# Optimization experiments

Measured on AMD Instinct MI355X. Metric: run time of the kernel, lower is better.

The kernel has to match this reference:

```python
import jax, jax.numpy as jnp
import numpy as np

N, F_IN, HID, NH1, NCLS = 8192, 256, 64, 4, 16
LRELU_ALPHA = 0.2  # tf.nn.leaky_relu default


def setup_inputs() -> dict:
    key = jax.random.key(0)
    ks = jax.random.split(key, 12)
    s = 0.05
    seq = jax.random.normal(ks[0], (1, N, F_IN), jnp.float32)
    # sparse-ish adjacency -> additive mask bias (0 on edges, -1e9 elsewhere)
    adj = jax.random.uniform(ks[1], (N, N)) < 0.005
    adj = adj | jnp.eye(N, dtype=bool)
    bias_mat = jnp.where(adj, 0.0, -1e9).astype(jnp.float32)[None]  # [1,N,N]
    return {
        "seq": seq,
        "bias_mat": bias_mat,
        "W1": jax.random.normal(ks[2], (NH1, F_IN, HID), jnp.float32) * s,
        "a1_src": jax.random.normal(ks[3], (NH1, HID, 1), jnp.float32) * s,
        "a1_dst": jax.random.normal(ks[4], (NH1, HID, 1), jnp.float32) * s,
        "b1_src": jnp.zeros((NH1, 1), jnp.float32),
        "b1_dst": jnp.zeros((NH1, 1), jnp.float32),
        "bias1": jnp.zeros((NH1, HID), jnp.float32),
        "W2": jax.random.normal(ks[5], (1, NH1 * HID, NCLS), jnp.float32) * s,
        "a2_src": jax.random.normal(ks[6], (1, NCLS, 1), jnp.float32) * s,
        "a2_dst": jax.random.normal(ks[7], (1, NCLS, 1), jnp.float32) * s,
        "b2_src": jnp.zeros((1, 1), jnp.float32),
        "b2_dst": jnp.zeros((1, 1), jnp.float32),
        "bias2": jnp.zeros((1, NCLS), jnp.float32),
    }


def _gat_layer(x, bias_mat, W, a_src, a_dst, b_src, b_dst, bias_out):
    # x: [N, Fin]; W: [nh, Fin, H]; bias_mat: [1, N, N]
    fts = jnp.einsum('nf,hfd->hnd', x, W)                      # Conv1D(k=1, no bias)
    f1 = jnp.einsum('hnd,hdo->hno', fts, a_src) + b_src[:, None, :]  # [nh,N,1]
    f2 = jnp.einsum('hnd,hdo->hno', fts, a_dst) + b_dst[:, None, :]  # [nh,N,1]
    logits = f1 + jnp.swapaxes(f2, 1, 2)                       # [nh,N,N]
    coefs = jax.nn.softmax(jax.nn.leaky_relu(logits, LRELU_ALPHA) + bias_mat, axis=-1)
    vals = jnp.einsum('hnm,hmd->hnd', coefs, fts)              # [nh,N,H]
    return vals + bias_out[:, None, :]


def reference(seq, bias_mat, W1, a1_src, a1_dst, b1_src, b1_dst, bias1,
              W2, a2_src, a2_dst, b2_src, b2_dst, bias2):
    x = seq[0]  # [N, F_IN]; batch dim is 1
    # layer 1: NH1 heads, elu activation, concat over heads
    h = jax.nn.elu(_gat_layer(x, bias_mat, W1, a1_src, a1_dst, b1_src, b1_dst, bias1))
    h1 = jnp.transpose(h, (1, 0, 2)).reshape(N, NH1 * HID)     # tf.concat(heads, -1)
    # output layer: 1 head, identity activation, averaged over final heads (=1)
    out = _gat_layer(h1, bias_mat, W2, a2_src, a2_dst, b2_src, b2_dst, bias2)
    logits = out[0] / 1.0                                      # add_n/final_sum
    return logits[None]  # [1, N, NCLS]
```

## Files before the change

### kernel.cpp

```cpp
#include <hip/hip_runtime.h>
#include <hip/hip_bf16.h>
#include <math.h>

#define NN    8192
#define FIN   256
#define HID   64
#define NH    4
#define NC    16
#define MAXD  128
#define ALPHA 0.2f
#define KC    32

typedef float nfloat4 __attribute__((ext_vector_type(4)));
__device__ __forceinline__ float4 ldnt4(const float4* p) {
    nfloat4 v = __builtin_nontemporal_load((const nfloat4*)p);
    return make_float4(v.x, v.y, v.z, v.w);
}
__device__ __forceinline__ ushort f2bf(float x) {
    __hip_bfloat16 h = __float2bfloat16(x);
    return *reinterpret_cast<ushort*>(&h);
}
__device__ __forceinline__ float bfhi(unsigned u) { return __uint_as_float(u & 0xffff0000u); }
__device__ __forceinline__ float bflo(unsigned u) { return __uint_as_float(u << 16); }

__device__ __forceinline__ void scan_row(
    int row, int lane, int* colsW,
    const float* __restrict__ bias, int* __restrict__ deg, int* __restrict__ cols)
{
    const unsigned long long lt = (1ull << lane) - 1ull;
    colsW[lane] = 0; colsW[64 + lane] = 0;
    const float4* rp = (const float4*)(bias + (size_t)row * NN);
    float4 vv[8];
    #pragma unroll
    for (int k = 0; k < 8; ++k) vv[k] = ldnt4(rp + k*64 + lane);
    int base = 0;
    #pragma unroll
    for (int s = 0; s < 4; ++s) {
        #pragma unroll
        for (int k = 0; k < 8; ++k) {
            const float4 v = vv[k];
            if (s < 3) vv[k] = ldnt4(rp + ((s+1)*8 + k)*64 + lane);
            const unsigned long long m0 = __ballot(v.x == 0.f);
            const unsigned long long m1 = __ballot(v.y == 0.f);
            const unsigned long long m2 = __ballot(v.z == 0.f);
            const unsigned long long m3 = __ballot(v.w == 0.f);
            const int cb = ((s*8 + k)*64 + lane)*4;
            int p = base + __popcll(m0&lt) + __popcll(m1&lt)
                         + __popcll(m2&lt) + __popcll(m3&lt);
            if (v.x == 0.f) { if (p < MAXD) colsW[p] = cb;     ++p; }
            if (v.y == 0.f) { if (p < MAXD) colsW[p] = cb + 1; ++p; }
            if (v.z == 0.f) { if (p < MAXD) colsW[p] = cb + 2; ++p; }
            if (v.w == 0.f) { if (p < MAXD) colsW[p] = cb + 3; ++p; }
            base += __popcll(m0) + __popcll(m1) + __popcll(m2) + __popcll(m3);
        }
    }
    const int d = base < MAXD ? base : MAXD;
    if (lane == 0) deg[row] = d;
    cols[(size_t)row*MAXD + lane]      = colsW[lane];
    cols[(size_t)row*MAXD + 64 + lane] = colsW[64 + lane];
}

__global__ __launch_bounds__(256) void k_gemm_scan(
    const float* __restrict__ seq, const float* __restrict__ W1,
    const float* __restrict__ a1s, const float* __restrict__ a1d,
    const float* __restrict__ b1s, const float* __restrict__ b1d,
    const float* __restrict__ bias,
    ushort* __restrict__ fts1g, float* __restrict__ f1v, float* __restrict__ f2v,
    int* __restrict__ deg, int* __restrict__ cols)
{
    __shared__ union {
        struct { float xsT[KC][68]; float w[KC][68]; } g;
        struct { float r1[64][17];  float r2[64][17]; } gr;
        int colsS[4][MAXD];
    } S;
    const int t = threadIdx.x, bid = blockIdx.x;
    const int w = t >> 6, lane = t & 63;

    const bool isGemm = (bid < 1024) && !(bid & 1);
    if (!isGemm) {
        const int si = (bid < 1024) ? (bid >> 1) : (bid - 512);
        scan_row(si*4 + w, lane, &S.colsS[w][0], bias, deg, cols);
        return;
    }
    const int gi = bid >> 1;
    const int head = gi & 3, rowbase = (gi >> 2) * 64;
    const int tr = t >> 4, tc = t & 15;

    float acc[4][4] = {};
    for (int kc = 0; kc < FIN / KC; ++kc) {
        #pragma unroll
        for (int i = 0; i < 2; ++i) {
            const int lin = t + i*256;
            const int row = lin >> 3, kq = lin & 7;
            const float4 v = *(const float4*)(seq + (size_t)(rowbase + row)*FIN + kc*KC + kq*4);
            S.g.xsT[kq*4+0][row] = v.x;
            S.g.xsT[kq*4+1][row] = v.y;
            S.g.xsT[kq*4+2][row] = v.z;
            S.g.xsT[kq*4+3][row] = v.w;
        }
        #pragma unroll
        for (int i = 0; i < 2; ++i) {
            const int lin = t + i*256;
            const int k = lin >> 4, dq = lin & 15;
            *(float4*)&S.g.w[k][dq*4] =
                *(const float4*)(W1 + ((size_t)head*FIN + kc*KC + k)*HID + dq*4);
        }
        __syncthreads();
        #pragma unroll 8
        for (int k = 0; k < KC; ++k) {
            const float4 aa = *(const float4*)&S.g.xsT[k][tr*4];
            const float4 bb = *(const float4*)&S.g.w[k][tc*4];
            acc[0][0] += aa.x*bb.x; acc[0][1] += aa.x*bb.y; acc[0][2] += aa.x*bb.z; acc[0][3] += aa.x*bb.w;
            acc[1][0] += aa.y*bb.x; acc[1][1] += aa.y*bb.y; acc[1][2] += aa.y*bb.z; acc[1][3] += aa.y*bb.w;
            acc[2][0] += aa.z*bb.x; acc[2][1] += aa.z*bb.y; acc[2][2] += aa.z*bb.z; acc[2][3] += aa.z*bb.w;
            acc[3][0] += aa.w*bb.x; acc[3][1] += aa.w*bb.y; acc[3][2] += aa.w*bb.z; acc[3][3] += aa.w*bb.w;
        }
        __syncthreads();
    }
    float p1[4], p2[4];
    #pragma unroll
    for (int i = 0; i < 4; ++i) {
        const int node = rowbase + tr*4 + i;
        ushort4 o;
        o.x = f2bf(acc[i][0]); o.y = f2bf(acc[i][1]);
        o.z = f2bf(acc[i][2]); o.w = f2bf(acc[i][3]);
        *(ushort4*)&fts1g[(size_t)node*(NH*HID) + head*HID + tc*4] = o;
        float s1 = 0.f, s2 = 0.f;
        #pragma unroll
        for (int j = 0; j < 4; ++j) {
            s1 += acc[i][j] * a1s[head*HID + tc*4 + j];
            s2 += acc[i][j] * a1d[head*HID + tc*4 + j];
        }
        p1[i] = s1; p2[i] = s2;
    }
    #pragma unroll
    for (int i = 0; i < 4; ++i) {
        S.gr.r1[tr*4 + i][tc] = p1[i];
        S.gr.r2[tr*4 + i][tc] = p2[i];
    }
    __syncthreads();
    if (t < 64) {
        float s1 = b1s[head], s2 = b1d[head];
        #pragma unroll
        for (int q = 0; q < 16; ++q) { s1 += S.gr.r1[t][q]; s2 += S.gr.r2[t][q]; }
        f1v[(rowbase + t)*NH + head] = s1;
        f2v[(rowbase + t)*NH + head] = s2;
    }
}

__global__ __launch_bounds__(256) void k_attn1(
    const ushort* __restrict__ fts1g, const float* __restrict__ f1v4,
    const float* __restrict__ f2v4, const float* __restrict__ bias1,
    const float* __restrict__ W2, const float* __restrict__ a2s,
    const float* __restrict__ a2d, const float* __restrict__ b2s,
    const float* __restrict__ b2d,
    const int* __restrict__ deg, const int* __restrict__ cols,
    float* __restrict__ fts2, float* __restrict__ g1, float* __restrict__ g2)
{
    __shared__ int    colsS[4][MAXD];
    __shared__ float4 coefS[4][MAXD];
    __shared__ float  h1S[4][NH*68];

    const int t = threadIdx.x, w = t >> 6, lane = t & 63;
    const int row = blockIdx.x*4 + w;
    int*    colsW = &colsS[w][0];
    float4* coefW = &coefS[w][0];
    float*  h1W   = &h1S[w][0];

    const int d = deg[row];
    const int c0 = cols[(size_t)row*MAXD + lane];
    const int c1 = cols[(size_t)row*MAXD + 64 + lane];
    colsW[lane] = c0; colsW[64 + lane] = c1;

    const float4 f1 = *(const float4*)(f1v4 + (size_t)row*NH);
    float4 s0 = make_float4(-1e30f,-1e30f,-1e30f,-1e30f), s1 = s0;
    if (lane < d) {
        const float4 F = *(const float4*)(f2v4 + (size_t)c0*NH);
        float x;
        x = f1.x + F.x; s0.x = x > 0.f ? x : ALPHA*x;
        x = f1.y + F.y; s0.y = x > 0.f ? x : ALPHA*x;
        x = f1.z + F.z; s0.z = x > 0.f ? x : ALPHA*x;
        x = f1.w + F.w; s0.w = x > 0.f ? x : ALPHA*x;
    }
    if (lane + 64 < d) {
        const float4 F = *(const float4*)(f2v4 + (size_t)c1*NH);
        float x;
        x = f1.x + F.x; s1.x = x > 0.f ? x : ALPHA*x;
        x = f1.y + F.y; s1.y = x > 0.f ? x : ALPHA*x;
        x = f1.z + F.z; s1.z = x > 0.f ? x : ALPHA*x;
        x = f1.w + F.w; s1.w = x > 0.f ? x : ALPHA*x;
    }
    float4 m;
    m.x = fmaxf(s0.x, s1.x); m.y = fmaxf(s0.y, s1.y);
    m.z = fmaxf(s0.z, s1.z); m.w = fmaxf(s0.w, s1.w);
    #pragma unroll
    for (int off = 32; off; off >>= 1) {
        m.x = fmaxf(m.x, __shfl_xor(m.x, off));
        m.y = fmaxf(m.y, __shfl_xor(m.y, off));
        m.z = fmaxf(m.z, __shfl_xor(m.z, off));
        m.w = fmaxf(m.w, __shfl_xor(m.w, off));
    }
    float4 p0 = make_float4(0,0,0,0), p1 = p0;
    if (lane < d) {
        p0.x = __expf(s0.x - m.x); p0.y = __expf(s0.y - m.y);
        p0.z = __expf(s0.z - m.z); p0.w = __expf(s0.w - m.w);
    }
    if (lane + 64 < d) {
        p1.x = __expf(s1.x - m.x); p1.y = __expf(s1.y - m.y);
        p1.z = __expf(s1.z - m.z); p1.w = __expf(s1.w - m.w);
    }
    coefW[lane] = p0; coefW[64 + lane] = p1;
    float4 sum;
    sum.x = p0.x + p1.x; sum.y = p0.y + p1.y;
    sum.z = p0.z + p1.z; sum.w = p0.w + p1.w;
    #pragma unroll
    for (int off = 32; off; off >>= 1) {
        sum.x += __shfl_xor(sum.x, off);
        sum.y += __shfl_xor(sum.y, off);
        sum.z += __shfl_xor(sum.z, off);
        sum.w += __shfl_xor(sum.w, off);
    }
    const int h = lane >> 4;
    const float invh = (h==0) ? 1.f/sum.x : (h==1) ? 1.f/sum.y
                     : (h==2) ? 1.f/sum.z : 1.f/sum.w;

    float a0 = 0.f, a1 = 0.f, a2 = 0.f, a3 = 0.f;
    #pragma unroll 8
    for (int e = 0; e < d; ++e) {
        const float4 q4 = coefW[e];
        const float cf = (h==0) ? q4.x : (h==1) ? q4.y : (h==2) ? q4.z : q4.w;
        const uint2 q = *(const uint2*)(fts1g + (size_t)colsW[e]*(NH*HID) + lane*4);
        a0 += cf * bflo(q.x); a1 += cf * bfhi(q.x);
        a2 += cf * bflo(q.y); a3 += cf * bfhi(q.y);
    }
    const float4 bv = *(const float4*)(bias1 + lane*4);
    float4 ev;
    float v;
    v = a0*invh + bv.x; ev.x = v > 0.f ? v : __expf(v) - 1.f;
    v = a1*invh + bv.y; ev.y = v > 0.f ? v : __expf(v) - 1.f;
    v = a2*invh + bv.z; ev.z = v > 0.f ? v : __expf(v) - 1.f;
    v = a3*invh + bv.w; ev.w = v > 0.f ? v : __expf(v) - 1.f;
    *(float4*)&h1W[h*68 + (lane & 15)*4] = ev;

    const int part = lane >> 4, c = lane & 15;
    float s = 0.f;
    #pragma unroll 8
    for (int q = 0; q < 64; ++q)
        s += h1W[part*68 + q] * W2[(part*64 + q)*NC + c];
    s += __shfl_xor(s, 16);
    s += __shfl_xor(s, 32);
    if (lane < NC) fts2[(size_t)row*NC + lane] = s;

    float t1 = (lane < NC) ? s * a2s[lane] : 0.f;
    float t2 = (lane < NC) ? s * a2d[lane] : 0.f;
    #pragma unroll
    for (int off = 8; off; off >>= 1) {
        t1 += __shfl_xor(t1, off);
        t2 += __shfl_xor(t2, off);
    }
    if (lane == 0) { g1[row] = t1 + b2s[0]; g2[row] = t2 + b2d[0]; }
}

__global__ __launch_bounds__(256) void k_attn2(
    const float* __restrict__ fts2, const float* __restrict__ g1,
    const float* __restrict__ g2, const float* __restrict__ bias2,
    const int* __restrict__ deg, const int* __restrict__ cols,
    float* __restrict__ out)
{
    __shared__ int   colsS[4][MAXD];
    __shared__ float coefS[4][MAXD];
    const int t = threadIdx.x, w = t >> 6, lane = t & 63;
    const int i = blockIdx.x*4 + w;
    const int d = deg[i];
    for (int e = lane; e < MAXD; e += 64) colsS[w][e] = (e < d) ? cols[(size_t)i*MAXD + e] : 0;

    const float g1i = g1[i];
    float sc0 = -1e30f, sc1 = -1e30f;
    if (lane < d)      { const float x = g1i + g2[colsS[w][lane]];    sc0 = x > 0.f ? x : ALPHA*x; }
    if (lane + 64 < d) { const float x = g1i + g2[colsS[w][lane+64]]; sc1 = x > 0.f ? x : ALPHA*x; }
    float m = fmaxf(sc0, sc1);
    #pragma unroll
    for (int off = 32; off; off >>= 1) m = fmaxf(m, __shfl_xor(m, off));
    const float p0 = (lane      < d) ? __expf(sc0 - m) : 0.f;
    const float p1 = (lane + 64 < d) ? __expf(sc1 - m) : 0.f;
    coefS[w][lane] = p0; coefS[w][lane + 64] = p1;
    float sum = p0 + p1;
    #pragma unroll
    for (int off = 32; off; off >>= 1) sum += __shfl_xor(sum, off);
    const float inv = 1.f / sum;

    const int eg = lane >> 4, c = lane & 15;
    float acc = 0.f;
    #pragma unroll 2
    for (int e0 = 0; e0 < d; e0 += 4) {
        const int e = e0 + eg;
        if (e < d) acc += coefS[w][e] * fts2[(size_t)colsS[w][e]*NC + c];
    }
    acc += __shfl_xor(acc, 16);
    acc += __shfl_xor(acc, 32);
    if (lane < NC) out[(size_t)i*NC + lane] = acc*inv + bias2[lane];
}

extern "C" void kernel_launch(void* const* d_in, const int* in_sizes, int n_in,
                              void* d_out, int out_size, void* d_ws, size_t ws_size,
                              hipStream_t stream)
{
    const float* seq   = (const float*)d_in[0];
    const float* bias  = (const float*)d_in[1];
    const float* W1    = (const float*)d_in[2];
    const float* a1s   = (const float*)d_in[3];
    const float* a1d   = (const float*)d_in[4];
    const float* b1s   = (const float*)d_in[5];
    const float* b1d   = (const float*)d_in[6];
    const float* bias1 = (const float*)d_in[7];
    const float* W2    = (const float*)d_in[8];
    const float* a2s   = (const float*)d_in[9];
    const float* a2d   = (const float*)d_in[10];
    const float* b2s   = (const float*)d_in[11];
    const float* b2d   = (const float*)d_in[12];
    const float* bias2 = (const float*)d_in[13];

    char* ws = (char*)d_ws;
    int*    deg   = (int*)ws;    ws += (size_t)NN * 4;
    int*    cols  = (int*)ws;    ws += (size_t)NN * MAXD * 4;
    ushort* fts1g = (ushort*)ws; ws += (size_t)NN * NH * HID * 2;
    float*  f1v   = (float*)ws;  ws += (size_t)NN * NH * 4;
    float*  f2v   = (float*)ws;  ws += (size_t)NN * NH * 4;
    float*  fts2  = (float*)ws;  ws += (size_t)NN * NC * 4;
    float*  g1    = (float*)ws;  ws += (size_t)NN * 4;
    float*  g2    = (float*)ws;  ws += (size_t)NN * 4;

    hipLaunchKernelGGL(k_gemm_scan, dim3(512 + NN/4), dim3(256), 0, stream,
                       seq, W1, a1s, a1d, b1s, b1d, bias,
                       fts1g, f1v, f2v, deg, cols);
    hipLaunchKernelGGL(k_attn1, dim3(NN/4), dim3(256), 0, stream,
                       fts1g, f1v, f2v, bias1, W2, a2s, a2d, b2s, b2d,
                       deg, cols, fts2, g1, g2);
    hipLaunchKernelGGL(k_attn2, dim3(NN/4), dim3(256), 0, stream,
                       fts2, g1, g2, bias2, deg, cols, (float*)d_out);
}
```

Measured before the change: 97.72 us.

## Fuse most adjacency scanning into first attention kernel, shrink gemm-scan grid

The first kernel now runs only the layer-1 GEMM and scans the first 2048 adjacency rows. The attention kernel scans the remaining rows itself and computes attention on them straight from shared memory, while a quarter of its blocks use the pre-scanned rows. The aim is to overlap the bandwidth-heavy scan of the bias matrix with the gather and compute of attention, and to avoid re-reading column lists. The cost is heavier, uneven blocks in the fused kernel, which may unbalance the load.

```diff
diff --git a/kernel.cpp b/kernel.cpp
--- a/kernel.cpp
+++ b/kernel.cpp
@@ -23,7 +23,7 @@
 __device__ __forceinline__ float bfhi(unsigned u) { return __uint_as_float(u & 0xffff0000u); }
 __device__ __forceinline__ float bflo(unsigned u) { return __uint_as_float(u << 16); }
 
-__device__ __forceinline__ void scan_row(
+__device__ __forceinline__ int scan_row(
     int row, int lane, int* colsW,
     const float* __restrict__ bias, int* __restrict__ deg, int* __restrict__ cols)
 {
@@ -58,6 +58,107 @@
     if (lane == 0) deg[row] = d;
     cols[(size_t)row*MAXD + lane]      = colsW[lane];
     cols[(size_t)row*MAXD + 64 + lane] = colsW[64 + lane];
+    return d;
+}
+
+__device__ __forceinline__ void attn_row(
+    int row, int lane, int d, int* colsW, float4* coefW, float* h1W,
+    const ushort* __restrict__ fts1g, const float* __restrict__ f1v4,
+    const float* __restrict__ f2v4, const float* __restrict__ bias1,
+    const float* __restrict__ W2, const float* __restrict__ a2s,
+    const float* __restrict__ a2d, const float* __restrict__ b2s,
+    const float* __restrict__ b2d,
+    float* __restrict__ fts2, float* __restrict__ g1, float* __restrict__ g2)
+{
+    const int c0 = colsW[lane], c1 = colsW[64 + lane];
+
+    const float4 f1 = *(const float4*)(f1v4 + (size_t)row*NH);
+    float4 s0 = make_float4(-1e30f,-1e30f,-1e30f,-1e30f), s1 = s0;
+    if (lane < d) {
+        const float4 F = *(const float4*)(f2v4 + (size_t)c0*NH);
+        float x;
+        x = f1.x + F.x; s0.x = x > 0.f ? x : ALPHA*x;
+        x = f1.y + F.y; s0.y = x > 0.f ? x : ALPHA*x;
+        x = f1.z + F.z; s0.z = x > 0.f ? x : ALPHA*x;
+        x = f1.w + F.w; s0.w = x > 0.f ? x : ALPHA*x;
+    }
+    if (lane + 64 < d) {
+        const float4 F = *(const float4*)(f2v4 + (size_t)c1*NH);
+        float x;
+        x = f1.x + F.x; s1.x = x > 0.f ? x : ALPHA*x;
+        x = f1.y + F.y; s1.y = x > 0.f ? x : ALPHA*x;
+        x = f1.z + F.z; s1.z = x > 0.f ? x : ALPHA*x;
+        x = f1.w + F.w; s1.w = x > 0.f ? x : ALPHA*x;
+    }
+    float4 m;
+    m.x = fmaxf(s0.x, s1.x); m.y = fmaxf(s0.y, s1.y);
+    m.z = fmaxf(s0.z, s1.z); m.w = fmaxf(s0.w, s1.w);
+    #pragma unroll
+    for (int off = 32; off; off >>= 1) {
+        m.x = fmaxf(m.x, __shfl_xor(m.x, off));
+        m.y = fmaxf(m.y, __shfl_xor(m.y, off));
+        m.z = fmaxf(m.z, __shfl_xor(m.z, off));
+        m.w = fmaxf(m.w, __shfl_xor(m.w, off));
+    }
+    float4 p0 = make_float4(0,0,0,0), p1 = p0;
+    if (lane < d) {
+        p0.x = __expf(s0.x - m.x); p0.y = __expf(s0.y - m.y);
+        p0.z = __expf(s0.z - m.z); p0.w = __expf(s0.w - m.w);
+    }
+    if (lane + 64 < d) {
+        p1.x = __expf(s1.x - m.x); p1.y = __expf(s1.y - m.y);
+        p1.z = __expf(s1.z - m.z); p1.w = __expf(s1.w - m.w);
+    }
+    coefW[lane] = p0; coefW[64 + lane] = p1;
+    float4 sum;
+    sum.x = p0.x + p1.x; sum.y = p0.y + p1.y;
+    sum.z = p0.z + p1.z; sum.w = p0.w + p1.w;
+    #pragma unroll
+    for (int off = 32; off; off >>= 1) {
+        sum.x += __shfl_xor(sum.x, off);
+        sum.y += __shfl_xor(sum.y, off);
+        sum.z += __shfl_xor(sum.z, off);
+        sum.w += __shfl_xor(sum.w, off);
+    }
+    const int h = lane >> 4;
+    const float invh = (h==0) ? 1.f/sum.x : (h==1) ? 1.f/sum.y
+                     : (h==2) ? 1.f/sum.z : 1.f/sum.w;
+
+    float a0 = 0.f, a1 = 0.f, a2 = 0.f, a3 = 0.f;
+    #pragma unroll 8
+    for (int e = 0; e < d; ++e) {
+        const float4 q4 = coefW[e];
+        const float cf = (h==0) ? q4.x : (h==1) ? q4.y : (h==2) ? q4.z : q4.w;
+        const uint2 q = *(const uint2*)(fts1g + (size_t)colsW[e]*(NH*HID) + lane*4);
+        a0 += cf * bflo(q.x); a1 += cf * bfhi(q.x);
+        a2 += cf * bflo(q.y); a3 += cf * bfhi(q.y);
+    }
+    const float4 bv = *(const float4*)(bias1 + lane*4);
+    float4 ev;
+    float v;
+    v = a0*invh + bv.x; ev.x = v > 0.f ? v : __expf(v) - 1.f;
+    v = a1*invh + bv.y; ev.y = v > 0.f ? v : __expf(v) - 1.f;
+    v = a2*invh + bv.z; ev.z = v > 0.f ? v : __expf(v) - 1.f;
+    v = a3*invh + bv.w; ev.w = v > 0.f ? v : __expf(v) - 1.f;
+    *(float4*)&h1W[h*68 + (lane & 15)*4] = ev;
+
+    const int part = lane >> 4, c = lane & 15;
+    float s = 0.f;
+    #pragma unroll 8
+    for (int q = 0; q < 64; ++q)
+        s += h1W[part*68 + q] * W2[(part*64 + q)*NC + c];
+    s += __shfl_xor(s, 16);
+    s += __shfl_xor(s, 32);
+    if (lane < NC) fts2[(size_t)row*NC + lane] = s;
+
+    float t1 = (lane < NC) ? s * a2s[lane] : 0.f;
+    float t2 = (lane < NC) ? s * a2d[lane] : 0.f;
+    #pragma unroll
+    for (int off = 8; off; off >>= 1) {
+        t1 += __shfl_xor(t1, off);
+        t2 += __shfl_xor(t2, off);
+    }
+    if (lane == 0) { g1[row] = t1 + b2s[0]; g2[row] = t2 + b2d[0]; }
 }
 
 __global__ __launch_bounds__(256) void k_gemm_scan(
@@ -76,14 +177,11 @@
     const int t = threadIdx.x, bid = blockIdx.x;
     const int w = t >> 6, lane = t & 63;
 
-    const bool isGemm = (bid < 1024) && !(bid & 1);
-    if (!isGemm) {
-        const int si = (bid < 1024) ? (bid >> 1) : (bid - 512);
-        scan_row(si*4 + w, lane, &S.colsS[w][0], bias, deg, cols);
+    if (bid >= 512) {
+        scan_row((bid - 512)*4 + w, lane, &S.colsS[w][0], bias, deg, cols);
         return;
     }
-    const int gi = bid >> 1;
-    const int head = gi & 3, rowbase = (gi >> 2) * 64;
+    const int head = bid & 3, rowbase = (bid >> 2) * 64;
     const int tr = t >> 4, tc = t & 15;
 
     float acc[4][4] = {};
@@ -148,117 +246,40 @@
     }
 }
 
-__global__ __launch_bounds__(256) void k_attn1(
-    const ushort* __restrict__ fts1g, const float* __restrict__ f1v4,
-    const float* __restrict__ f2v4, const float* __restrict__ bias1,
-    const float* __restrict__ W2, const float* __restrict__ a2s,
-    const float* __restrict__ a2d, const float* __restrict__ b2s,
-    const float* __restrict__ b2d,
-    const int* __restrict__ deg, const int* __restrict__ cols,
+__global__ __launch_bounds__(256) void k_fused(
+    const float* __restrict__ bias, const ushort* __restrict__ fts1g,
+    const float* __restrict__ f1v4, const float* __restrict__ f2v4,
+    const float* __restrict__ bias1, const float* __restrict__ W2,
+    const float* __restrict__ a2s, const float* __restrict__ a2d,
+    const float* __restrict__ b2s, const float* __restrict__ b2d,
+    int* __restrict__ deg, int* __restrict__ cols,
     float* __restrict__ fts2, float* __restrict__ g1, float* __restrict__ g2)
 {
     __shared__ int    colsS[4][MAXD];
     __shared__ float4 coefS[4][MAXD];
     __shared__ float  h1S[4][NH*68];
 
-    const int t = threadIdx.x, w = t >> 6, lane = t & 63;
-    const int row = blockIdx.x*4 + w;
+    const int t = threadIdx.x, bid = blockIdx.x;
+    const int w = t >> 6, lane = t & 63;
     int*    colsW = &colsS[w][0];
     float4* coefW = &coefS[w][0];
     float*  h1W   = &h1S[w][0];
 
-    const int d = deg[row];
-    const int c0 = cols[(size_t)row*MAXD + lane];
-    const int c1 = cols[(size_t)row*MAXD + 64 + lane];
-    colsW[lane] = c0; colsW[64 + lane] = c1;
-
-    const float4 f1 = *(const float4*)(f1v4 + (size_t)row*NH);
-    float4 s0 = make_float4(-1e30f,-1e30f,-1e30f,-1e30f), s1 = s0;
-    if (lane < d) {
-        const float4 F = *(const float4*)(f2v4 + (size_t)c0*NH);
-        float x;
-        x = f1.x + F.x; s0.x = x > 0.f ? x : ALPHA*x;
-        x = f1.y + F.y; s0.y = x > 0.f ? x : ALPHA*x;
-        x = f1.z + F.z; s0.z = x > 0.f ? x : ALPHA*x;
-        x = f1.w + F.w; s0.w = x > 0.f ? x : ALPHA*x;
-    }
-    if (lane + 64 < d) {
-        const float4 F = *(const float4*)(f2v4 + (size_t)c1*NH);
-        float x;
-        x = f1.x + F.x; s1.x = x > 0.f ? x : ALPHA*x;
-        x = f1.y + F.y; s1.y = x > 0.f ? x : ALPHA*x;
-        x = f1.z + F.z; s1.z = x > 0.f ? x : ALPHA*x;
-        x = f1.w + F.w; s1.w = x > 0.f ? x : ALPHA*x;
-    }
-    float4 m;
-    m.x = fmaxf(s0.x, s1.x); m.y = fmaxf(s0.y, s1.y);
-    m.z = fmaxf(s0.z, s1.z); m.w = fmaxf(s0.w, s1.w);
-    #pragma unroll
-    for (int off = 32; off; off >>= 1) {
-        m.x = fmaxf(m.x, __shfl_xor(m.x, off));
-        m.y = fmaxf(m.y, __shfl_xor(m.y, off));
-        m.z = fmaxf(m.z, __shfl_xor(m.z, off));
-        m.w = fmaxf(m.w, __shfl_xor(m.w, off));
-    }
-    float4 p0 = make_float4(0,0,0,0), p1 = p0;
-    if (lane < d) {
-        p0.x = __expf(s0.x - m.x); p0.y = __expf(s0.y - m.y);
-        p0.z = __expf(s0.z - m.z); p0.w = __expf(s0.w - m.w);
-    }
-    if (lane + 64 < d) {
-        p1.x = __expf(s1.x - m.x); p1.y = __expf(s1.y - m.y);
-        p1.z = __expf(s1.z - m.z); p1.w = __expf(s1.w - m.w);
-    }
-    coefW[lane] = p0; coefW[64 + lane] = p1;
-    float4 sum;
-    sum.x = p0.x + p1.x; sum.y = p0.y + p1.y;
-    sum.z = p0.z + p1.z; sum.w = p0.w + p1.w;
-    #pragma unroll
-    for (int off = 32; off; off >>= 1) {
-        sum.x += __shfl_xor(sum.x, off);
-        sum.y += __shfl_xor(sum.y, off);
-        sum.z += __shfl_xor(sum.z, off);
-        sum.w += __shfl_xor(sum.w, off);
-    }
-    const int h = lane >> 4;
-    const float invh = (h==0) ? 1.f/sum.x : (h==1) ? 1.f/sum.y
-                     : (h==2) ? 1.f/sum.z : 1.f/sum.w;
-
-    float a0 = 0.f, a1 = 0.f, a2 = 0.f, a3 = 0.f;
-    #pragma unroll 8
-    for (int e = 0; e < d; ++e) {
-        const float4 q4 = coefW[e];
-        const float cf = (h==0) ? q4.x : (h==1) ? q4.y : (h==2) ? q4.z : q4.w;
-        const uint2 q = *(const uint2*)(fts1g + (size_t)colsW[e]*(NH*HID) + lane*4);
-        a0 += cf * bflo(q.x); a1 += cf * bfhi(q.x);
-        a2 += cf * bflo(q.y); a3 += cf * bfhi(q.y);
-    }
-    const float4 bv = *(const float4*)(bias1 + lane*4);
-    float4 ev;
-    float v;
-    v = a0*invh + bv.x; ev.x = v > 0.f ? v : __expf(v) - 1.f;
-    v = a1*invh + bv.y; ev.y = v > 0.f ? v : __expf(v) - 1.f;
-    v = a2*invh + bv.z; ev.z = v > 0.f ? v : __expf(v) - 1.f;
-    v = a3*invh + bv.w; ev.w = v > 0.f ? v : __expf(v) - 1.f;
-    *(float4*)&h1W[h*68 + (lane & 15)*4] = ev;
-
-    const int part = lane >> 4, c = lane & 15;
-    float s = 0.f;
-    #pragma unroll 8
-    for (int q = 0; q < 64; ++q)
-        s += h1W[part*68 + q] * W2[(part*64 + q)*NC + c];
-    s += __shfl_xor(s, 16);
-    s += __shfl_xor(s, 32);
-    if (lane < NC) fts2[(size_t)row*NC + lane] = s;
-
-    float t1 = (lane < NC) ? s * a2s[lane] : 0.f;
-    float t2 = (lane < NC) ? s * a2d[lane] : 0.f;
-    #pragma unroll
-    for (int off = 8; off; off >>= 1) {
-        t1 += __shfl_xor(t1, off);
-        t2 += __shfl_xor(t2, off);
-    }
-    if (lane == 0) { g1[row] = t1 + b2s[0]; g2[row] = t2 + b2d[0]; }
+    const int q = bid >> 2, r = bid & 3;
+    int row, d;
+    if (r == 3) {
+        row = q*4 + w;
+        d = deg[row];
+        colsW[lane]      = cols[(size_t)row*MAXD + lane];
+        colsW[64 + lane] = cols[(size_t)row*MAXD + 64 + lane];
+    } else {
+        const int f = q*3 + r;
+        row = 2048 + f*4 + w;
+        d = scan_row(row, lane, colsW, bias, deg, cols);
+    }
+    attn_row(row, lane, d, colsW, coefW, h1W,
+             fts1g, f1v4, f2v4, bias1, W2, a2s, a2d, b2s, b2d,
+             fts2, g1, g2);
 }
 
 __global__ __launch_bounds__(256) void k_attn2(
@@ -330,11 +351,11 @@
     float*  g1    = (float*)ws;  ws += (size_t)NN * 4;
     float*  g2    = (float*)ws;  ws += (size_t)NN * 4;
 
-    hipLaunchKernelGGL(k_gemm_scan, dim3(512 + NN/4), dim3(256), 0, stream,
+    hipLaunchKernelGGL(k_gemm_scan, dim3(1024), dim3(256), 0, stream,
                        seq, W1, a1s, a1d, b1s, b1d, bias,
                        fts1g, f1v, f2v, deg, cols);
-    hipLaunchKernelGGL(k_attn1, dim3(NN/4), dim3(256), 0, stream,
-                       fts1g, f1v, f2v, bias1, W2, a2s, a2d, b2s, b2d,
+    hipLaunchKernelGGL(k_fused, dim3(2048), dim3(256), 0, stream,
+                       bias, fts1g, f1v, f2v, bias1, W2, a2s, a2d, b2s, b2d,
                        deg, cols, fts2, g1, g2);
     hipLaunchKernelGGL(k_attn2, dim3(NN/4), dim3(256), 0, stream,
                        fts2, g1, g2, bias2, deg, cols, (float*)d_out);
```

Measured after the change: 101.6 us. 1.04x slower.

## Split each attention row across two waves and reorder gemm/scan block mapping

Applied to the files above, without the earlier changes.

k_attn1 now assigns two wavefronts per row, each handling alternating edges, and merges the softmax max, sum and aggregated features through shared memory with block barriers. This halves the serial per-wave gather loop over neighbors and doubles the number of waves doing the gather. It adds three __syncthreads and leaves half the waves idle in the epilogue. The gemm/scan kernel also places all gemm blocks first instead of interleaving them with scan blocks.

```diff
diff --git a/kernel.cpp b/kernel.cpp
--- a/kernel.cpp
+++ b/kernel.cpp
@@ -76,14 +76,11 @@
     const int t = threadIdx.x, bid = blockIdx.x;
     const int w = t >> 6, lane = t & 63;
 
-    const bool isGemm = (bid < 1024) && !(bid & 1);
-    if (!isGemm) {
-        const int si = (bid < 1024) ? (bid >> 1) : (bid - 512);
-        scan_row(si*4 + w, lane, &S.colsS[w][0], bias, deg, cols);
+    if (bid >= 512) {
+        scan_row((bid - 512)*4 + w, lane, &S.colsS[w][0], bias, deg, cols);
         return;
     }
-    const int gi = bid >> 1;
-    const int head = gi & 3, rowbase = (gi >> 2) * 64;
+    const int head = bid & 3, rowbase = (bid >> 2) * 64;
     const int tr = t >> 4, tc = t & 15;
 
     float acc[4][4] = {};
@@ -157,42 +154,34 @@
     const int* __restrict__ deg, const int* __restrict__ cols,
     float* __restrict__ fts2, float* __restrict__ g1, float* __restrict__ g2)
 {
-    __shared__ int    colsS[4][MAXD];
-    __shared__ float4 coefS[4][MAXD];
-    __shared__ float  h1S[4][NH*68];
+    __shared__ int    colsS[2][MAXD];
+    __shared__ float4 coefS[2][MAXD];
+    __shared__ float4 mS[2][2];
+    __shared__ float4 sS[2][2];
+    __shared__ float4 accS[2][64];
+    __shared__ float  h1S[2][NH*68];
 
     const int t = threadIdx.x, w = t >> 6, lane = t & 63;
-    const int row = blockIdx.x*4 + w;
-    int*    colsW = &colsS[w][0];
-    float4* coefW = &coefS[w][0];
-    float*  h1W   = &h1S[w][0];
+    const int rw = w >> 1, half = w & 1;
+    const int row = blockIdx.x*2 + rw;
+    const int h = lane >> 4;
 
     const int d = deg[row];
-    const int c0 = cols[(size_t)row*MAXD + lane];
-    const int c1 = cols[(size_t)row*MAXD + 64 + lane];
-    colsW[lane] = c0; colsW[64 + lane] = c1;
-
+    colsS[rw][half*64 + lane] = cols[(size_t)row*MAXD + half*64 + lane];
+    __syncthreads();
+
+    const int e0 = 2*lane + half;
     const float4 f1 = *(const float4*)(f1v4 + (size_t)row*NH);
-    float4 s0 = make_float4(-1e30f,-1e30f,-1e30f,-1e30f), s1 = s0;
-    if (lane < d) {
-        const float4 F = *(const float4*)(f2v4 + (size_t)c0*NH);
+    float4 s0 = make_float4(-1e30f,-1e30f,-1e30f,-1e30f);
+    if (e0 < d) {
+        const float4 F = *(const float4*)(f2v4 + (size_t)colsS[rw][e0]*NH);
         float x;
         x = f1.x + F.x; s0.x = x > 0.f ? x : ALPHA*x;
         x = f1.y + F.y; s0.y = x > 0.f ? x : ALPHA*x;
         x = f1.z + F.z; s0.z = x > 0.f ? x : ALPHA*x;
         x = f1.w + F.w; s0.w = x > 0.f ? x : ALPHA*x;
     }
-    if (lane + 64 < d) {
-        const float4 F = *(const float4*)(f2v4 + (size_t)c1*NH);
-        float x;
-        x = f1.x + F.x; s1.x = x > 0.f ? x : ALPHA*x;
-        x = f1.y + F.y; s1.y = x > 0.f ? x : ALPHA*x;
-        x = f1.z + F.z; s1.z = x > 0.f ? x : ALPHA*x;
-        x = f1.w + F.w; s1.w = x > 0.f ? x : ALPHA*x;
-    }
-    float4 m;
-    m.x = fmaxf(s0.x, s1.x); m.y = fmaxf(s0.y, s1.y);
-    m.z = fmaxf(s0.z, s1.z); m.w = fmaxf(s0.w, s1.w);
+    float4 m = s0;
     #pragma unroll
     for (int off = 32; off; off >>= 1) {
         m.x = fmaxf(m.x, __shfl_xor(m.x, off));
@@ -200,19 +189,20 @@
         m.z = fmaxf(m.z, __shfl_xor(m.z, off));
         m.w = fmaxf(m.w, __shfl_xor(m.w, off));
     }
-    float4 p0 = make_float4(0,0,0,0), p1 = p0;
-    if (lane < d) {
-        p0.x = __expf(s0.x - m.x); p0.y = __expf(s0.y - m.y);
-        p0.z = __expf(s0.z - m.z); p0.w = __expf(s0.w - m.w);
-    }
-    if (lane + 64 < d) {
-        p1.x = __expf(s1.x - m.x); p1.y = __expf(s1.y - m.y);
-        p1.z = __expf(s1.z - m.z); p1.w = __expf(s1.w - m.w);
-    }
-    coefW[lane] = p0; coefW[64 + lane] = p1;
-    float4 sum;
-    sum.x = p0.x + p1.x; sum.y = p0.y + p1.y;
-    sum.z = p0.z + p1.z; sum.w = p0.w + p1.w;
+    if (lane == 0) mS[rw][half] = m;
+    __syncthreads();
+    {
+        const float4 mA = mS[rw][0], mB = mS[rw][1];
+        m.x = fmaxf(mA.x, mB.x); m.y = fmaxf(mA.y, mB.y);
+        m.z = fmaxf(mA.z, mB.z); m.w = fmaxf(mA.w, mB.w);
+    }
+    float4 p = make_float4(0,0,0,0);
+    if (e0 < d) {
+        p.x = __expf(s0.x - m.x); p.y = __expf(s0.y - m.y);
+        p.z = __expf(s0.z - m.z); p.w = __expf(s0.w - m.w);
+    }
+    coefS[rw][e0] = p;
+    float4 sum = p;
     #pragma unroll
     for (int off = 32; off; off >>= 1) {
         sum.x += __shfl_xor(sum.x, off);
@@ -220,18 +210,32 @@
         sum.z += __shfl_xor(sum.z, off);
         sum.w += __shfl_xor(sum.w, off);
     }
-    const int h = lane >> 4;
+    if (lane == 0) sS[rw][half] = sum;
+    __syncthreads();
+    {
+        const float4 sA = sS[rw][0], sB = sS[rw][1];
+        sum.x = sA.x + sB.x; sum.y = sA.y + sB.y;
+        sum.z = sA.z + sB.z; sum.w = sA.w + sB.w;
+    }
     const float invh = (h==0) ? 1.f/sum.x : (h==1) ? 1.f/sum.y
                      : (h==2) ? 1.f/sum.z : 1.f/sum.w;
 
     float a0 = 0.f, a1 = 0.f, a2 = 0.f, a3 = 0.f;
     #pragma unroll 8
-    for (int e = 0; e < d; ++e) {
-        const float4 q4 = coefW[e];
+    for (int e = half; e < d; e += 2) {
+        const float4 q4 = coefS[rw][e];
         const float cf = (h==0) ? q4.x : (h==1) ? q4.y : (h==2) ? q4.z : q4.w;
-        const uint2 q = *(const uint2*)(fts1g + (size_t)colsW[e]*(NH*HID) + lane*4);
+        const uint2 q = *(const uint2*)(fts1g + (size_t)colsS[rw][e]*(NH*HID) + lane*4);
         a0 += cf * bflo(q.x); a1 += cf * bfhi(q.x);
         a2 += cf * bflo(q.y); a3 += cf * bfhi(q.y);
+    }
+    if (half == 1) accS[rw][lane] = make_float4(a0, a1, a2, a3);
+    __syncthreads();
+    if (half == 1) return;
+
+    {
+        const float4 o = accS[rw][lane];
+        a0 += o.x; a1 += o.y; a2 += o.z; a3 += o.w;
     }
     const float4 bv = *(const float4*)(bias1 + lane*4);
     float4 ev;
@@ -240,13 +244,13 @@
     v = a1*invh + bv.y; ev.y = v > 0.f ? v : __expf(v) - 1.f;
     v = a2*invh + bv.z; ev.z = v > 0.f ? v : __expf(v) - 1.f;
     v = a3*invh + bv.w; ev.w = v > 0.f ? v : __expf(v) - 1.f;
-    *(float4*)&h1W[h*68 + (lane & 15)*4] = ev;
+    *(float4*)&h1S[rw][h*68 + (lane & 15)*4] = ev;
 
     const int part = lane >> 4, c = lane & 15;
     float s = 0.f;
     #pragma unroll 8
     for (int q = 0; q < 64; ++q)
-        s += h1W[part*68 + q] * W2[(part*64 + q)*NC + c];
+        s += h1S[rw][part*68 + q] * W2[(part*64 + q)*NC + c];
     s += __shfl_xor(s, 16);
     s += __shfl_xor(s, 32);
     if (lane < NC) fts2[(size_t)row*NC + lane] = s;
@@ -333,7 +337,7 @@
     hipLaunchKernelGGL(k_gemm_scan, dim3(512 + NN/4), dim3(256), 0, stream,
                        seq, W1, a1s, a1d, b1s, b1d, bias,
                        fts1g, f1v, f2v, deg, cols);
-    hipLaunchKernelGGL(k_attn1, dim3(NN/4), dim3(256), 0, stream,
+    hipLaunchKernelGGL(k_attn1, dim3(NN/2), dim3(256), 0, stream,
                        fts1g, f1v, f2v, bias1, W2, a2s, a2d, b2s, b2d,
                        deg, cols, fts2, g1, g2);
     hipLaunchKernelGGL(k_attn2, dim3(NN/4), dim3(256), 0, stream,
```

New measurement: 97.50 us. No clear change (-0.2%).
